# Performance work log

Measured on AMD Instinct MI355X. Metric: run time of the kernel, lower is better.

Reference implementation:

```python
import jax, jax.numpy as jnp
import numpy as np

N_NODES = 10000
N_EDGES = 160000
MUL = 16            # multiplicity: emb_dim=64, max_l=1 -> irreps 16x0e + 16x1o
EMB = 64
NUM_BASIS = 10
MAX_RADIUS = 4.5
HIDDEN = 64
N_PATHS = 4         # (0e,0e->0e), (0e,1o->1o), (1o,0e->1o), (1o,1o->0e)
W_NUMEL = N_PATHS * MUL * MUL  # 1024


def setup_inputs() -> dict:
    key = jax.random.key(0)
    ks = jax.random.split(key, 6)
    x = jax.random.normal(ks[0], (N_NODES, EMB), jnp.float32)
    src = jax.random.randint(ks[1], (N_EDGES,), 0, N_NODES)
    dst = jax.random.randint(ks[2], (N_EDGES,), 0, N_NODES)
    edge_vec = jax.random.normal(ks[3], (N_EDGES, 3), jnp.float32)
    mlp_w1 = jax.random.normal(ks[4], (NUM_BASIS, HIDDEN), jnp.float32)
    mlp_w2 = jax.random.normal(ks[5], (HIDDEN, W_NUMEL), jnp.float32)
    return {"x": x, "edge_vec": edge_vec, "mlp_w1": mlp_w1,
            "mlp_w2": mlp_w2, "src": src, "dst": dst}


def _sus(t):
    # e3nn smooth bump helper: exp(-1/t) for t>0 else 0
    return jnp.where(t > 0, jnp.exp(-1.0 / jnp.where(t > 0, t, 1.0)), 0.0)


def _radial_embedding(r):
    # soft_one_hot_linspace(basis='smooth_finite', cutoff=True), then *sqrt(num_basis)
    values = jnp.linspace(0.0, MAX_RADIUS, NUM_BASIS + 2)[1:-1]
    step = MAX_RADIUS / (NUM_BASIS + 1)
    diff = (r[:, None] - values) / step                     # [E, NUM_BASIS]
    basis = 1.14136 * jnp.exp(2.0) * _sus(diff + 1.0) * _sus(1.0 - diff)
    return basis * (NUM_BASIS ** 0.5)


def _forward(x, edge_vec, mlp_w1, mlp_w2, src, dst):
    E = edge_vec.shape[0]
    N = x.shape[0]
    r = jnp.linalg.norm(edge_vec, axis=1)                   # [E]
    # spherical harmonics, lmax=1, normalize=True, 'component' norm: Y0=1, Y1=sqrt(3)*n
    y1 = jnp.sqrt(3.0) * edge_vec / r[:, None]              # [E, 3]

    # radial MLP (e3nn FullyConnectedNet: W~N(0,1), x@W/sqrt(fan_in), relu scaled by sqrt(2))
    emb = _radial_embedding(r)                              # [E, 10]
    h = jnp.sqrt(2.0) * jax.nn.relu(emb @ (mlp_w1 / NUM_BASIS ** 0.5))
    w = h @ (mlp_w2 / HIDDEN ** 0.5)                        # [E, 1024]
    w = w.reshape(E, N_PATHS, MUL, MUL)                     # paths in e3nn order A,B,C,D

    xs = x[src]                                             # gather [E, 64]
    x0 = xs[:, :MUL]                                        # [E, 16] 0e scalars
    x1 = xs[:, MUL:].reshape(E, MUL, 3)                     # [E, 16, 3] 1o vectors

    # Fully connected TP normalization ('component', path_norm 'element'):
    # out0 fan = 2*MUL -> alpha 1/(2*MUL); out1 alpha 3/(2*MUL) with w3j 1/sqrt(3)
    c = 1.0 / jnp.sqrt(2.0 * MUL)
    inv_sqrt3 = 1.0 / jnp.sqrt(3.0)
    wA, wB, wC, wD = w[:, 0], w[:, 1], w[:, 2], w[:, 3]
    # 0e outputs: 0e*0e->0e and 1o*1o->0e (dot product, w3j = I/sqrt(3))
    out0 = c * (jnp.einsum('euw,eu->ew', wA, x0)
                + inv_sqrt3 * jnp.einsum('euw,eum,em->ew', wD, x1, y1))
    # 1o outputs: 0e*1o->1o and 1o*0e->1o (w3j = I/sqrt(3), Y0 = 1)
    out1 = c * (jnp.einsum('euw,eu,em->ewm', wB, x0, y1)
                + jnp.einsum('euw,eum->ewm', wC, x1))
    summand = jnp.concatenate([out0, out1.reshape(E, MUL * 3)], axis=1)  # [E, 64]

    out = jax.ops.segment_sum(summand, dst, num_segments=N)             # [N, 64]
    return out * (N / E)


def reference(x, edge_vec, mlp_w1, mlp_w2, src, dst):
    return _forward(x, edge_vec, mlp_w1, mlp_w2, src, dst)
```

## Files before the change

### kernel.cpp

```cpp
#include <hip/hip_runtime.h>
#include <hip/hip_bf16.h>


typedef __attribute__((ext_vector_type(8))) short bf16x8;
typedef __attribute__((ext_vector_type(4))) float f32x4;

#define NN 10000
#define NE 160000

__device__ __forceinline__ float sus_f(float t) { return t > 0.0f ? __expf(-1.0f / t) : 0.0f; }
__device__ __forceinline__ unsigned int f2bf(float f) {
    unsigned int u = __float_as_uint(f);
    u += 0x7FFFu + ((u >> 16) & 1u);
    return u >> 16;
}
__device__ __forceinline__ float bf2f(unsigned short v) { return __uint_as_float(((unsigned int)v) << 16); }

#define GL16(g, l) __builtin_amdgcn_global_load_lds( \
    (const __attribute__((address_space(1))) void*)(g), \
    (__attribute__((address_space(3))) void*)(l), 16, 0, 0)

__device__ __forceinline__ void stage_lds(const void* g, void* l, int bytes, int wv, int lane) {
    const char* gc = (const char*)g;
    char* lc = (char*)l;
    const int units = bytes >> 4;
    for (int u0 = wv << 6; u0 < units; u0 += 512) {
        if (u0 + lane < units) GL16(gc + (((long)(u0 + lane)) << 4), lc + (u0 << 4));
    }
}

__global__ void hist_k(const int* __restrict__ dst, int* __restrict__ hist,
                       const float* __restrict__ w2, char* __restrict__ w2bf) {
    if (blockIdx.x < 625) {
        const int e = blockIdx.x * 256 + threadIdx.x;
        if (e < NE) atomicAdd(&hist[dst[e]], 1);
    } else {
        const int idx = (blockIdx.x - 625) * 256 + threadIdx.x;
        const int j = idx >> 10, R = idx & 1023;
        unsigned int pk[4];
        #pragma unroll
        for (int p = 0; p < 4; ++p) {
            const unsigned int lo = f2bf(w2[(size_t)(8 * j + 2 * p) * 1024 + R]);
            const unsigned int hi = f2bf(w2[(size_t)(8 * j + 2 * p + 1) * 1024 + R]);
            pk[p] = lo | (hi << 16);
        }
        uint4 v; v.x = pk[0]; v.y = pk[1]; v.z = pk[2]; v.w = pk[3];
        *(uint4*)(w2bf + R * 128 + ((j ^ (R & 7)) << 4)) = v;
    }
}

__global__ __launch_bounds__(1024) void scan_k(const int* __restrict__ hist,
                                               int* __restrict__ offsets) {
    __shared__ int hl[NN];
    __shared__ int wsum[16];
    const int tid = threadIdx.x;
    for (int i = tid; i < NN; i += 1024) hl[i] = hist[i];
    __syncthreads();
    const int base = tid * 10;
    int loc[10]; int s = 0;
    #pragma unroll
    for (int i = 0; i < 10; ++i) { loc[i] = s; const int b = base + i; s += (b < NN) ? hl[b] : 0; }
    int v = s;
    const int lane = tid & 63, wv = tid >> 6;
    #pragma unroll
    for (int d = 1; d < 64; d <<= 1) { int t2 = __shfl_up(v, d); if (lane >= d) v += t2; }
    if (lane == 63) wsum[wv] = v;
    __syncthreads();
    if (tid < 64) {
        int w = (tid < 16) ? wsum[tid] : 0;
        #pragma unroll
        for (int d = 1; d < 16; d <<= 1) { int t2 = __shfl_up(w, d); if (tid >= d) w += t2; }
        if (tid < 16) wsum[tid] = w;
    }
    __syncthreads();
    const int wexc = (wv == 0) ? 0 : wsum[wv - 1];
    const int texc = wexc + v - s;
    #pragma unroll
    for (int i = 0; i < 10; ++i) { const int b = base + i; if (b < NN) offsets[b] = texc + loc[i]; }
    if (tid == 1023) offsets[NN] = texc + s;
}

__global__ void scatter_k(const int* __restrict__ dst, const int* __restrict__ offsets,
                          int* __restrict__ cursor, int* __restrict__ perm,
                          int* __restrict__ dsts) {
    const int e = blockIdx.x * 256 + threadIdx.x;
    if (e < NE) {
        const int d = dst[e];
        const int pos = offsets[d] + atomicAdd(&cursor[d], 1);
        perm[pos] = e;
        dsts[pos] = d;
    }
}

__global__ __launch_bounds__(256, 4) void prep_k(
    const float* __restrict__ x, const float* __restrict__ edge_vec,
    const float* __restrict__ w1, const int* __restrict__ src,
    const int* __restrict__ perm,
    char* __restrict__ h_bf, char* __restrict__ X0g, char* __restrict__ Zg,
    char* __restrict__ X1g, float* __restrict__ Y1g)
{
    __shared__ float embl[128][10];
    __shared__ float y1l[128][4];
    __shared__ int srcl[128];
    __shared__ float w1l[640];
    const int tid = threadIdx.x;
    const long e0 = (long)blockIdx.x * 128;

    for (int i = tid; i < 640; i += 256) w1l[i] = w1[i];
    if (tid < 128) {
        const int e = tid;
        const int eid = perm[e0 + e];
        const float vx = edge_vec[eid * 3 + 0];
        const float vy = edge_vec[eid * 3 + 1];
        const float vz = edge_vec[eid * 3 + 2];
        const float r = sqrtf(vx * vx + vy * vy + vz * vz);
        const float sc = 1.7320508075688772f / r;
        y1l[e][0] = vx * sc; y1l[e][1] = vy * sc; y1l[e][2] = vz * sc; y1l[e][3] = 0.f;
        *(float4*)&Y1g[(e0 + e) * 4] = make_float4(vx * sc, vy * sc, vz * sc, 0.f);
        srcl[e] = src[eid];
        const float C0 = 1.14136f * __expf(2.0f) * 3.1622776601683795f;
        #pragma unroll
        for (int i = 0; i < 10; ++i) {
            const float diff = r * (11.0f / 4.5f) - (float)(i + 1);
            embl[e][i] = C0 * sus_f(diff + 1.0f) * sus_f(1.0f - diff);
        }
    }
    __syncthreads();
    for (int idx = tid; idx < 1024; idx += 256) {
        const int e = idx >> 3, j = idx & 7;
        float acc[8];
        #pragma unroll
        for (int jj = 0; jj < 8; ++jj) acc[jj] = 0.0f;
        #pragma unroll
        for (int i = 0; i < 10; ++i) {
            const float ei = embl[e][i];
            #pragma unroll
            for (int jj = 0; jj < 8; ++jj) acc[jj] += ei * w1l[i * 64 + j * 8 + jj];
        }
        unsigned int pk[4];
        #pragma unroll
        for (int p = 0; p < 4; ++p) {
            const unsigned int lo = f2bf(fmaxf(acc[2 * p],     0.0f) * 0.4472135954999579f);
            const unsigned int hi = f2bf(fmaxf(acc[2 * p + 1], 0.0f) * 0.4472135954999579f);
            pk[p] = lo | (hi << 16);
        }
        uint4 v; v.x = pk[0]; v.y = pk[1]; v.z = pk[2]; v.w = pk[3];
        *(uint4*)(h_bf + (e0 + e) * 128 + ((j ^ (e & 7)) << 4)) = v;
    }
    for (int idx = tid; idx < 1024; idx += 256) {
        const int e = idx >> 3, p = idx & 7;
        const int s = srcl[e];
        const float2 ab = *(const float2*)&x[(size_t)s * 64 + 2 * p];
        *(unsigned int*)(X0g + (e0 + e) * 36 + p * 4) = f2bf(ab.x) | (f2bf(ab.y) << 16);
    }
    for (int idx = tid; idx < 1024; idx += 256) {
        const int e = idx >> 3, p = idx & 7;
        const int s = srcl[e];
        const float* xp = x + (size_t)s * 64 + 16 + 6 * p;
        const float z0 = xp[0] * y1l[e][0] + xp[1] * y1l[e][1] + xp[2] * y1l[e][2];
        const float z1 = xp[3] * y1l[e][0] + xp[4] * y1l[e][1] + xp[5] * y1l[e][2];
        *(unsigned int*)(Zg + (e0 + e) * 36 + p * 4) = f2bf(z0) | (f2bf(z1) << 16);
    }
    for (int idx = tid; idx < 128 * 12; idx += 256) {
        const int e = idx / 12, qd = idx - e * 12;
        const int s = srcl[e];
        const float4 v = *(const float4*)&x[(size_t)s * 64 + 16 + 4 * qd];
        *(float4*)(X1g + (e0 + e) * 208 + qd * 16) = v;
    }
}

#define BUF_SZ 48128

__global__ __launch_bounds__(512, 2) void se3_edge2(
    const char* __restrict__ w2bf, const char* __restrict__ h_bf,
    const char* __restrict__ X0g, const char* __restrict__ Zg,
    const char* __restrict__ X1g, const float* __restrict__ Y1g,
    const int* __restrict__ dsts, float* __restrict__ out)
{
    __shared__ __align__(16) char w2lds[65536];
    __shared__ __align__(16) char bufs[2][BUF_SZ];
    __shared__ int segst[2][66];
    __shared__ int nseg[2];

    const int tid = threadIdx.x, lane = tid & 63, wv = tid >> 6;
    const int lm = lane & 15, q = lane >> 4;
    const int bx = blockIdx.x;
    const int pair = (bx & 1) ^ ((bx >> 8) & 1);
    const int tb = bx >> 1;
    const int s0 = (q ^ (lm & 7)) << 4;
    const int s1 = s0 ^ 64;
    const int erow = wv << 4;

    const char* w2p0 = w2lds;
    const char* w2p1 = w2lds + 32768;
    {
        const int pa = pair ? 1 : 0, pb = pair ? 2 : 3;
        stage_lds(w2bf + pa * 32768, w2lds, 32768, wv, lane);
        stage_lds(w2bf + pb * 32768, w2lds + 32768, 32768, wv, lane);
        const long e0 = (long)tb * 5 * 128;
        stage_lds(h_bf + e0 * 128, bufs[0], 16384, wv, lane);
        stage_lds(X0g + e0 * 36, bufs[0] + 16384, 4608, wv, lane);
        if (pair) stage_lds(X1g + e0 * 208, bufs[0] + 20992, 26624, wv, lane);
        else      stage_lds(Zg  + e0 * 36,  bufs[0] + 20992, 4608,  wv, lane);
        stage_lds((const char*)(dsts + e0), bufs[0] + 47616, 512, wv, lane);
    }
    __syncthreads();

    const float S = 0.17677669529663687f * 0.125f * 0.0625f;

    for (int tt = 0; tt < 5; ++tt) {
        char* buf = bufs[tt & 1];
        const long gt = (long)tb * 5 + tt;
        const long e0 = gt * 128;
        if (tt < 4) {
            char* nb = bufs[(tt & 1) ^ 1];
            const long ne0 = e0 + 128;
            stage_lds(h_bf + ne0 * 128, nb, 16384, wv, lane);
            stage_lds(X0g + ne0 * 36, nb + 16384, 4608, wv, lane);
            if (pair) stage_lds(X1g + ne0 * 208, nb + 20992, 26624, wv, lane);
            else      stage_lds(Zg  + ne0 * 36,  nb + 20992, 4608,  wv, lane);
            stage_lds((const char*)(dsts + ne0), nb + 47616, 512, wv, lane);
        }
        const char* hl = buf;
        const int arow = erow + lm;
        const bf16x8 a0 = *(const bf16x8*)(hl + arow * 128 + s0);
        const bf16x8 a1 = *(const bf16x8*)(hl + arow * 128 + s1);
        const unsigned short* X0l = (const unsigned short*)(buf + 16384);
        const int* dstl = (const int*)(buf + 47616);

        float ac0[4] = {0,0,0,0}, ac1[4] = {0,0,0,0}, ac2[4] = {0,0,0,0}, ac3[4] = {0,0,0,0};

        if (pair == 0) {
            const unsigned short* Zl = (const unsigned short*)(buf + 20992);
            #pragma unroll 4
            for (int t = 0; t < 16; ++t) {
                const int rowb = (t * 16 + lm) << 7;
                const bf16x8 b00 = *(const bf16x8*)(w2p0 + rowb + s0);
                const bf16x8 b01 = *(const bf16x8*)(w2p0 + rowb + s1);
                const bf16x8 b10 = *(const bf16x8*)(w2p1 + rowb + s0);
                const bf16x8 b11 = *(const bf16x8*)(w2p1 + rowb + s1);
                f32x4 wA = {0.f,0.f,0.f,0.f};
                wA = __builtin_amdgcn_mfma_f32_16x16x32_bf16(a0, b00, wA, 0,0,0);
                wA = __builtin_amdgcn_mfma_f32_16x16x32_bf16(a1, b01, wA, 0,0,0);
                f32x4 wD = {0.f,0.f,0.f,0.f};
                wD = __builtin_amdgcn_mfma_f32_16x16x32_bf16(a0, b10, wD, 0,0,0);
                wD = __builtin_amdgcn_mfma_f32_16x16x32_bf16(a1, b11, wD, 0,0,0);
                #pragma unroll
                for (int r = 0; r < 4; ++r) {
                    const int el = erow + 4 * q + r;
                    ac0[r] += wA[r] * bf2f(X0l[el * 18 + t]);
                    ac1[r] += wD[r] * bf2f(Zl[el * 18 + t]);
                }
            }
            float* summ32 = (float*)buf;
            #pragma unroll
            for (int r = 0; r < 4; ++r) {
                const int el = erow + 4 * q + r;
                summ32[el * 17 + lm] = S * (ac0[r] + 0.5773502691896258f * ac1[r]);
            }
        } else {
            const float* X1l = (const float*)(buf + 20992);
            #pragma unroll 4
            for (int t = 0; t < 16; ++t) {
                const int rowb = (t * 16 + lm) << 7;
                const bf16x8 b00 = *(const bf16x8*)(w2p0 + rowb + s0);
                const bf16x8 b01 = *(const bf16x8*)(w2p0 + rowb + s1);
                const bf16x8 b10 = *(const bf16x8*)(w2p1 + rowb + s0);
                const bf16x8 b11 = *(const bf16x8*)(w2p1 + rowb + s1);
                f32x4 wB = {0.f,0.f,0.f,0.f};
                wB = __builtin_amdgcn_mfma_f32_16x16x32_bf16(a0, b00, wB, 0,0,0);
                wB = __builtin_amdgcn_mfma_f32_16x16x32_bf16(a1, b01, wB, 0,0,0);
                f32x4 wC = {0.f,0.f,0.f,0.f};
                wC = __builtin_amdgcn_mfma_f32_16x16x32_bf16(a0, b10, wC, 0,0,0);
                wC = __builtin_amdgcn_mfma_f32_16x16x32_bf16(a1, b11, wC, 0,0,0);
                #pragma unroll
                for (int r = 0; r < 4; ++r) {
                    const int el = erow + 4 * q + r;
                    ac0[r] += wB[r] * bf2f(X0l[el * 18 + t]);
                    ac1[r] += wC[r] * X1l[el * 52 + 3 * t + 0];
                    ac2[r] += wC[r] * X1l[el * 52 + 3 * t + 1];
                    ac3[r] += wC[r] * X1l[el * 52 + 3 * t + 2];
                }
            }
            unsigned short* summ16 = (unsigned short*)buf;
            #pragma unroll
            for (int r = 0; r < 4; ++r) {
                const int el = erow + 4 * q + r;
                const float4 y = *(const float4*)&Y1g[(e0 + el) * 4];
                const float b = S * ac0[r];
                summ16[el * 49 + 3 * lm + 0] = (unsigned short)f2bf(b * y.x + S * ac1[r]);
                summ16[el * 49 + 3 * lm + 1] = (unsigned short)f2bf(b * y.y + S * ac2[r]);
                summ16[el * 49 + 3 * lm + 2] = (unsigned short)f2bf(b * y.z + S * ac3[r]);
            }
        }
        if (wv < 2) {
            const int base = wv << 6;
            const int d = dstl[base + lane];
            const bool flag = (lane == 0) || (d != dstl[base + lane - 1]);
            const unsigned long long m = __ballot(flag);
            const int sid = (lane == 0) ? 0 : __popcll(m & ((1ull << lane) - 1ull));
            if (flag) segst[wv][sid] = base + lane;
            if (lane == 63) { const int ns = __popcll(m); nseg[wv] = ns; segst[wv][ns] = base + 64; }
        }
        __syncthreads();
        const int nsa = nseg[0], nsb = nseg[1];
        if (pair == 0) {
            const float* summ32 = (const float*)buf;
            const int total = (nsa + nsb) * 16;
            for (int i = tid; i < total; i += 512) {
                const int sg = i >> 4, c = i & 15;
                const int hh = sg >= nsa;
                const int sl = hh ? sg - nsa : sg;
                const int eb = segst[hh][sl], ee = segst[hh][sl + 1];
                float sum = 0.f;
                for (int e = eb; e < ee; ++e) sum += summ32[e * 17 + c];
                atomicAdd(&out[(size_t)dstl[eb] * 64 + c], sum);
            }
        } else {
            const unsigned short* summ16 = (const unsigned short*)buf;
            const int total = (nsa + nsb) * 48;
            for (int i = tid; i < total; i += 512) {
                const int sg = i / 48, c = i - sg * 48;
                const int hh = sg >= nsa;
                const int sl = hh ? sg - nsa : sg;
                const int eb = segst[hh][sl], ee = segst[hh][sl + 1];
                float sum = 0.f;
                for (int e = eb; e < ee; ++e) sum += bf2f(summ16[e * 49 + c]);
                atomicAdd(&out[(size_t)dstl[eb] * 64 + 16 + c], sum);
            }
        }
        __syncthreads();
    }
}

#define FBT 64
template<int PATH>
__device__ __forceinline__ void fb_body(
    const float* __restrict__ x, const float* __restrict__ edge_vec,
    const float* __restrict__ w1, const float* __restrict__ w2,
    const int* __restrict__ src, const int* __restrict__ perm,
    const int* __restrict__ dsts, float* __restrict__ out,
    unsigned short (*w2t)[72], float* arena, float (*y1l)[4],
    int* dstl, int* srcl, int* segstart, int* nseg_s)
{
    constexpr int NC    = (PATH == 0 || PATH == 3) ? 16 : 48;
    constexpr int CBASE = (PATH == 0 || PATH == 3) ? 0 : 16;
    const int tid = threadIdx.x;
    float* embl = arena;
    unsigned short* hl = (unsigned short*)(arena + 640);
    float* feats = arena + 2944;
    float* summ  = arena;
    {
        const float* col = w2 + PATH * 256 + tid;
        #pragma unroll
        for (int k = 0; k < 64; k += 2) {
            const unsigned int lo = f2bf(col[(size_t)k * 1024]);
            const unsigned int hi = f2bf(col[(size_t)(k + 1) * 1024]);
            *(unsigned int*)&w2t[tid][k] = lo | (hi << 16);
        }
    }
    const int lane = tid & 63, wv = tid >> 6, lm = lane & 15, q = lane >> 4;
    const int erow = wv * 16;
    const float C0 = 1.14136f * __expf(2.0f) * 3.1622776601683795f;
    const float S  = 0.17677669529663687f * 0.125f * 0.0625f;
    for (int it = 0; it < 2; ++it) {
        const int e0 = (blockIdx.x * 2 + it) * FBT;
        __syncthreads();
        for (int idx = tid; idx < FBT * 10; idx += 256) {
            const int e = idx / 10, i = idx - e * 10;
            const int eid = perm[e0 + e];
            const float vx = edge_vec[eid * 3 + 0], vy = edge_vec[eid * 3 + 1], vz = edge_vec[eid * 3 + 2];
            const float r = sqrtf(vx * vx + vy * vy + vz * vz);
            const float diff = r * (11.0f / 4.5f) - (float)(i + 1);
            embl[e * 10 + i] = C0 * sus_f(diff + 1.0f) * sus_f(1.0f - diff);
            if (i == 0) {
                const float sc = 1.7320508075688772f / r;
                y1l[e][0] = vx * sc; y1l[e][1] = vy * sc; y1l[e][2] = vz * sc;
                dstl[e] = dsts[e0 + e];
                srcl[e] = src[eid];
            }
        }
        __syncthreads();
        for (int idx = tid; idx < FBT * 8; idx += 256) {
            const int e = idx >> 3, j0 = (idx & 7) * 8;
            float acc[8];
            #pragma unroll
            for (int j = 0; j < 8; ++j) acc[j] = 0.0f;
            #pragma unroll
            for (int i = 0; i < 10; ++i) {
                const float ei = embl[e * 10 + i];
                #pragma unroll
                for (int j = 0; j < 8; ++j) acc[j] += ei * w1[i * 64 + j0 + j];
            }
            unsigned int pk[4];
            #pragma unroll
            for (int p = 0; p < 4; ++p) {
                const unsigned int lo = f2bf(fmaxf(acc[2 * p],     0.0f) * 0.4472135954999579f);
                const unsigned int hi = f2bf(fmaxf(acc[2 * p + 1], 0.0f) * 0.4472135954999579f);
                pk[p] = lo | (hi << 16);
            }
            uint4 v; v.x = pk[0]; v.y = pk[1]; v.z = pk[2]; v.w = pk[3];
            *(uint4*)&hl[e * 72 + j0] = v;
        }
        if (PATH == 2) {
            for (int idx = tid; idx < FBT * 48; idx += 256) {
                const int e = idx / 48, c = idx - e * 48;
                feats[e * 48 + c] = x[(size_t)srcl[e] * 64 + 16 + c];
            }
        } else if (PATH == 3) {
            for (int idx = tid; idx < FBT * 16; idx += 256) {
                const int e = idx >> 4, u = idx & 15;
                const float* xs = x + (size_t)srcl[e] * 64 + 16 + u * 3;
                feats[e * 16 + u] = xs[0] * y1l[e][0] + xs[1] * y1l[e][1] + xs[2] * y1l[e][2];
            }
        } else {
            for (int idx = tid; idx < FBT * 16; idx += 256) {
                const int e = idx >> 4, u = idx & 15;
                feats[e * 16 + u] = x[(size_t)srcl[e] * 64 + u];
            }
        }
        __syncthreads();
        const bf16x8 a0 = *(const bf16x8*)&hl[(erow + lm) * 72 + 8 * q];
        const bf16x8 a1 = *(const bf16x8*)&hl[(erow + lm) * 72 + 32 + 8 * q];
        float accO[4] = {0.f,0.f,0.f,0.f}, accC0[4] = {0.f,0.f,0.f,0.f};
        float accC1[4] = {0.f,0.f,0.f,0.f}, accC2[4] = {0.f,0.f,0.f,0.f};
        #pragma unroll 4
        for (int t = 0; t < 16; ++t) {
            const bf16x8 b0 = *(const bf16x8*)&w2t[t * 16 + lm][8 * q];
            const bf16x8 b1 = *(const bf16x8*)&w2t[t * 16 + lm][32 + 8 * q];
            f32x4 wa = {0.f,0.f,0.f,0.f};
            wa = __builtin_amdgcn_mfma_f32_16x16x32_bf16(a0, b0, wa, 0, 0, 0);
            wa = __builtin_amdgcn_mfma_f32_16x16x32_bf16(a1, b1, wa, 0, 0, 0);
            #pragma unroll
            for (int r = 0; r < 4; ++r) {
                const int el = erow + 4 * q + r;
                if (PATH == 2) {
                    accC0[r] += wa[r] * feats[el * 48 + t * 3 + 0];
                    accC1[r] += wa[r] * feats[el * 48 + t * 3 + 1];
                    accC2[r] += wa[r] * feats[el * 48 + t * 3 + 2];
                } else {
                    accO[r] += wa[r] * feats[el * 16 + t];
                }
            }
        }
        __syncthreads();
        #pragma unroll
        for (int r = 0; r < 4; ++r) {
            const int el = erow + 4 * q + r;
            if (PATH == 0) summ[el * 16 + lm] = S * accO[r];
            else if (PATH == 3) summ[el * 16 + lm] = S * 0.5773502691896258f * accO[r];
            else if (PATH == 1) {
                const float tv = S * accO[r];
                summ[el * 48 + lm * 3 + 0] = tv * y1l[el][0];
                summ[el * 48 + lm * 3 + 1] = tv * y1l[el][1];
                summ[el * 48 + lm * 3 + 2] = tv * y1l[el][2];
            } else {
                summ[el * 48 + lm * 3 + 0] = S * accC0[r];
                summ[el * 48 + lm * 3 + 1] = S * accC1[r];
                summ[el * 48 + lm * 3 + 2] = S * accC2[r];
            }
        }
        if (tid < 64) {
            const int d = dstl[tid];
            const bool flag = (tid == 0) || (d != dstl[tid - 1]);
            const unsigned long long m = __ballot(flag);
            const int sid = (tid == 0) ? 0 : __popcll(m & ((1ull << tid) - 1ull));
            if (flag) segstart[sid] = tid;
            if (tid == 63) { const int ns = __popcll(m); *nseg_s = ns; segstart[ns] = 64; }
        }
        __syncthreads();
        const int ns = *nseg_s;
        for (int i = tid; i < ns * NC; i += 256) {
            const int s = i / NC, c = i - s * NC;
            const int eb = segstart[s], ee = segstart[s + 1];
            float sum = 0.0f;
            for (int e = eb; e < ee; ++e) sum += summ[e * NC + c];
            atomicAdd(&out[(size_t)dstl[eb] * 64 + CBASE + c], sum);
        }
    }
}

__global__ __launch_bounds__(256, 2) void fb_edge(
    const float* __restrict__ x, const float* __restrict__ edge_vec,
    const float* __restrict__ w1, const float* __restrict__ w2,
    const int* __restrict__ src, const int* __restrict__ perm,
    const int* __restrict__ dsts, float* __restrict__ out)
{
    __shared__ unsigned short w2t[256][72];
    __shared__ float arena[6016];
    __shared__ float y1l[FBT][4];
    __shared__ int dstl[FBT];
    __shared__ int srcl[FBT];
    __shared__ int segstart[FBT + 1];
    __shared__ int nseg_s;
    switch (blockIdx.y) {
        case 0:  fb_body<0>(x, edge_vec, w1, w2, src, perm, dsts, out, w2t, arena, y1l, dstl, srcl, segstart, &nseg_s); break;
        case 1:  fb_body<1>(x, edge_vec, w1, w2, src, perm, dsts, out, w2t, arena, y1l, dstl, srcl, segstart, &nseg_s); break;
        case 2:  fb_body<2>(x, edge_vec, w1, w2, src, perm, dsts, out, w2t, arena, y1l, dstl, srcl, segstart, &nseg_s); break;
        default: fb_body<3>(x, edge_vec, w1, w2, src, perm, dsts, out, w2t, arena, y1l, dstl, srcl, segstart, &nseg_s); break;
    }
}

extern "C" void kernel_launch(void* const* d_in, const int* in_sizes, int n_in,
                              void* d_out, int out_size, void* d_ws, size_t ws_size,
                              hipStream_t stream) {
    const float* x        = (const float*)d_in[0];
    const float* edge_vec = (const float*)d_in[1];
    const float* w1       = (const float*)d_in[2];
    const float* w2       = (const float*)d_in[3];
    const int*   src      = (const int*)d_in[4];
    const int*   dst      = (const int*)d_in[5];
    float* out = (float*)d_out;

    char* ws = (char*)d_ws;
    size_t off = 0;
    auto alloc = [&](size_t n) -> char* {
        off = (off + 255) & ~(size_t)255;
        char* p = ws + off; off += n; return p;
    };
    int* hist    = (int*)alloc(40000);
    int* cursor  = (int*)alloc(40000);
    int* offsets = (int*)alloc(40004);
    int* perm    = (int*)alloc(640000);
    int* dsts    = (int*)alloc(640000);
    char* w2bf   = alloc(131072);
    char* h_bf   = alloc((size_t)NE * 128);
    char* X0g    = alloc((size_t)NE * 36);
    char* Zg     = alloc((size_t)NE * 36);
    float* Y1g   = (float*)alloc((size_t)NE * 16);
    char* X1g    = alloc((size_t)NE * 208);
    const bool big = (off <= ws_size);

    hipMemsetAsync(d_out, 0, (size_t)out_size * sizeof(float), stream);
    hipMemsetAsync(d_ws, 0, 81408, stream);

    if (big) {
        hipLaunchKernelGGL(hist_k, dim3(657), dim3(256), 0, stream, dst, hist, w2, w2bf);
        hipLaunchKernelGGL(scan_k, dim3(1), dim3(1024), 0, stream, hist, offsets);
        hipLaunchKernelGGL(scatter_k, dim3(625), dim3(256), 0, stream, dst, offsets, cursor, perm, dsts);
        hipLaunchKernelGGL(prep_k, dim3(1250), dim3(256), 0, stream,
                           x, edge_vec, w1, src, perm, h_bf, X0g, Zg, X1g, Y1g);
        hipLaunchKernelGGL(se3_edge2, dim3(500), dim3(512), 0, stream,
                           w2bf, h_bf, X0g, Zg, X1g, Y1g, dsts, out);
    } else {
        hipLaunchKernelGGL(hist_k, dim3(625), dim3(256), 0, stream, dst, hist, w2, w2bf);
        hipLaunchKernelGGL(scan_k, dim3(1), dim3(1024), 0, stream, hist, offsets);
        hipLaunchKernelGGL(scatter_k, dim3(625), dim3(256), 0, stream, dst, offsets, cursor, perm, dsts);
        hipLaunchKernelGGL(fb_edge, dim3(1250, 4), dim3(256), 0, stream,
                           x, edge_vec, w1, w2, src, perm, dsts, out);
    }
}
```

Measured before the change: 126.8 us.

## Fuse scatter into prep, compact staged layouts, split edge kernel across 1024 threads

Removes the separate scatter kernel: prep now iterates edges in original order, computes each edge's sorted position with an atomic cursor and writes its per-edge data directly to that position. The staged per-edge buffers lose their padding (X0/Z at 32 bytes, X1 stored as bf16 at 128 bytes), and Y1 is staged into LDS. The main edge kernel goes from 512 to 1024 threads per block, splitting the 16 weight tiles across two wave halves with an LDS reduction before the segmented atomic scatter. This cuts global traffic and a launch, at the cost of scattered writes in prep, an extra barrier round, and bf16 rounding of X1.

```diff
diff --git a/kernel.cpp b/kernel.cpp
--- a/kernel.cpp
+++ b/kernel.cpp
@@ -3,6 +3,7 @@
 
 
 typedef __attribute__((ext_vector_type(8))) short bf16x8;
+typedef __attribute__((ext_vector_type(8))) unsigned short u16x8;
 typedef __attribute__((ext_vector_type(4))) float f32x4;
 
 #define NN 10000
@@ -15,18 +16,19 @@
     return u >> 16;
 }
 __device__ __forceinline__ float bf2f(unsigned short v) { return __uint_as_float(((unsigned int)v) << 16); }
+__device__ __forceinline__ float bflo(unsigned int v) { return __uint_as_float(v << 16); }
+__device__ __forceinline__ float bfhi(unsigned int v) { return __uint_as_float(v & 0xFFFF0000u); }
+__device__ __forceinline__ float bfe(u16x8 v, int i) { return __uint_as_float(((unsigned int)v[i]) << 16); }
 
 #define GL16(g, l) __builtin_amdgcn_global_load_lds( \
     (const __attribute__((address_space(1))) void*)(g), \
     (__attribute__((address_space(3))) void*)(l), 16, 0, 0)
 
-__device__ __forceinline__ void stage_lds(const void* g, void* l, int bytes, int wv, int lane) {
+__device__ __forceinline__ void stageN(const void* g, void* l, int bytes, int tid, int nthr) {
     const char* gc = (const char*)g;
     char* lc = (char*)l;
     const int units = bytes >> 4;
-    for (int u0 = wv << 6; u0 < units; u0 += 512) {
-        if (u0 + lane < units) GL16(gc + (((long)(u0 + lane)) << 4), lc + (u0 << 4));
-    }
+    for (int u = tid; u < units; u += nthr) GL16(gc + ((long)u << 4), lc + (u << 4));
 }
 
 __global__ void hist_k(const int* __restrict__ dst, int* __restrict__ hist,
@@ -80,6 +82,288 @@
     if (tid == 1023) offsets[NN] = texc + s;
 }
 
+__global__ __launch_bounds__(256, 4) void prep_k(
+    const float* __restrict__ x, const float* __restrict__ edge_vec,
+    const float* __restrict__ w1, const int* __restrict__ src,
+    const int* __restrict__ dst, const int* __restrict__ offsets,
+    int* __restrict__ cursor, int* __restrict__ dsts,
+    char* __restrict__ h_bf, char* __restrict__ X0g, char* __restrict__ Zg,
+    char* __restrict__ X1g, float* __restrict__ Y1g)
+{
+    __shared__ float embl[128][10];
+    __shared__ float y1l[128][4];
+    __shared__ int srcl[128];
+    __shared__ int posl[128];
+    __shared__ float w1l[640];
+    const int tid = threadIdx.x;
+    const int e0 = blockIdx.x * 128;
+
+    for (int i = tid; i < 640; i += 256) w1l[i] = w1[i];
+    if (tid < 128) {
+        const int eid = e0 + tid;
+        const int d = dst[eid];
+        const int pos = offsets[d] + atomicAdd(&cursor[d], 1);
+        posl[tid] = pos;
+        dsts[pos] = d;
+        const float vx = edge_vec[eid * 3 + 0];
+        const float vy = edge_vec[eid * 3 + 1];
+        const float vz = edge_vec[eid * 3 + 2];
+        const float r = sqrtf(vx * vx + vy * vy + vz * vz);
+        const float sc = 1.7320508075688772f / r;
+        y1l[tid][0] = vx * sc; y1l[tid][1] = vy * sc; y1l[tid][2] = vz * sc; y1l[tid][3] = 0.f;
+        *(float4*)&Y1g[(size_t)pos * 4] = make_float4(vx * sc, vy * sc, vz * sc, 0.f);
+        srcl[tid] = src[eid];
+        const float C0 = 1.14136f * __expf(2.0f) * 3.1622776601683795f;
+        #pragma unroll
+        for (int i = 0; i < 10; ++i) {
+            const float diff = r * (11.0f / 4.5f) - (float)(i + 1);
+            embl[tid][i] = C0 * sus_f(diff + 1.0f) * sus_f(1.0f - diff);
+        }
+    }
+    __syncthreads();
+    for (int idx = tid; idx < 1024; idx += 256) {
+        const int e = idx >> 3, j = idx & 7;
+        float acc[8];
+        #pragma unroll
+        for (int jj = 0; jj < 8; ++jj) acc[jj] = 0.0f;
+        #pragma unroll
+        for (int i = 0; i < 10; ++i) {
+            const float ei = embl[e][i];
+            #pragma unroll
+            for (int jj = 0; jj < 8; ++jj) acc[jj] += ei * w1l[i * 64 + j * 8 + jj];
+        }
+        unsigned int pk[4];
+        #pragma unroll
+        for (int p = 0; p < 4; ++p) {
+            const unsigned int lo = f2bf(fmaxf(acc[2 * p],     0.0f) * 0.4472135954999579f);
+            const unsigned int hi = f2bf(fmaxf(acc[2 * p + 1], 0.0f) * 0.4472135954999579f);
+            pk[p] = lo | (hi << 16);
+        }
+        const int pos = posl[e];
+        uint4 v; v.x = pk[0]; v.y = pk[1]; v.z = pk[2]; v.w = pk[3];
+        *(uint4*)(h_bf + (size_t)pos * 128 + ((j ^ (pos & 7)) << 4)) = v;
+    }
+    for (int idx = tid; idx < 1024; idx += 256) {
+        const int e = idx >> 3, p = idx & 7;
+        const int s = srcl[e];
+        const float2 ab = *(const float2*)&x[(size_t)s * 64 + 2 * p];
+        *(unsigned int*)(X0g + (size_t)posl[e] * 32 + p * 4) = f2bf(ab.x) | (f2bf(ab.y) << 16);
+    }
+    for (int idx = tid; idx < 1024; idx += 256) {
+        const int e = idx >> 3, p = idx & 7;
+        const int s = srcl[e];
+        const float* xp = x + (size_t)s * 64 + 16 + 6 * p;
+        const float z0 = xp[0] * y1l[e][0] + xp[1] * y1l[e][1] + xp[2] * y1l[e][2];
+        const float z1 = xp[3] * y1l[e][0] + xp[4] * y1l[e][1] + xp[5] * y1l[e][2];
+        *(unsigned int*)(Zg + (size_t)posl[e] * 32 + p * 4) = f2bf(z0) | (f2bf(z1) << 16);
+    }
+    for (int idx = tid; idx < 2048; idx += 256) {
+        const int e = idx >> 4, u = idx & 15;
+        const int s = srcl[e];
+        const float* xp = x + (size_t)s * 64 + 16 + 3 * u;
+        uint2 v;
+        v.x = f2bf(xp[0]) | (f2bf(xp[1]) << 16);
+        v.y = f2bf(xp[2]);
+        *(uint2*)(X1g + (size_t)posl[e] * 128 + u * 8) = v;
+    }
+}
+
+#define BUF 43520
+
+__global__ __launch_bounds__(1024, 4) void se3_edge3(
+    const char* __restrict__ w2bf, const char* __restrict__ h_bf,
+    const char* __restrict__ X0g, const char* __restrict__ Zg,
+    const char* __restrict__ X1g, const float* __restrict__ Y1g,
+    const int* __restrict__ dsts, float* __restrict__ out)
+{
+    __shared__ __align__(16) char w2lds[65536];
+    __shared__ __align__(16) char bufs[2][BUF];
+    __shared__ int segst[2][66];
+    __shared__ int nseg[2];
+
+    const int tid = threadIdx.x, lane = tid & 63, wv = tid >> 6;
+    const int lm = lane & 15, q = lane >> 4;
+    const int g = wv & 7, th = wv >> 3;
+    const int erow = g << 4;
+    const int bx = blockIdx.x;
+    const int pair = bx & 1;
+    const int tb = bx >> 1;
+    const int s0 = (q ^ (lm & 7)) << 4;
+    const int s1 = s0 ^ 64;
+
+    const char* w2p0 = w2lds;
+    const char* w2p1 = w2lds + 32768;
+
+    auto stage_tile = [&](char* nb, long e0) {
+        stageN(h_bf + e0 * 128, nb, 16384, tid, 1024);
+        stageN(X0g + e0 * 32, nb + 16384, 4096, tid, 1024);
+        if (pair) {
+            stageN(X1g + e0 * 128, nb + 24576, 16384, tid, 1024);
+            stageN((const char*)(Y1g + e0 * 4), nb + 40960, 2048, tid, 1024);
+        } else {
+            stageN(Zg + e0 * 32, nb + 20480, 4096, tid, 1024);
+        }
+        stageN((const char*)(dsts + e0), nb + 43008, 512, tid, 1024);
+    };
+
+    {
+        const int pa = pair ? 1 : 0, pb = pair ? 2 : 3;
+        stageN(w2bf + pa * 32768, w2lds, 32768, tid, 1024);
+        stageN(w2bf + pb * 32768, w2lds + 32768, 32768, tid, 1024);
+        stage_tile(bufs[0], (long)tb * 5 * 128);
+    }
+    __syncthreads();
+
+    const float S = 0.17677669529663687f * 0.125f * 0.0625f;
+
+    for (int tt = 0; tt < 5; ++tt) {
+        char* buf = bufs[tt & 1];
+        const long e0 = ((long)tb * 5 + tt) * 128;
+        if (tt < 4) stage_tile(bufs[(tt & 1) ^ 1], e0 + 128);
+
+        const int arow = erow + lm;
+        const bf16x8 a0 = *(const bf16x8*)(buf + arow * 128 + s0);
+        const bf16x8 a1 = *(const bf16x8*)(buf + arow * 128 + s1);
+        u16x8 x0r[4], zr[4];
+        #pragma unroll
+        for (int r = 0; r < 4; ++r) {
+            const int el = erow + 4 * q + r;
+            x0r[r] = *(const u16x8*)(buf + 16384 + el * 32 + th * 16);
+            if (pair == 0) zr[r] = *(const u16x8*)(buf + 20480 + el * 32 + th * 16);
+        }
+
+        float ac0[4] = {0,0,0,0}, ac1[4] = {0,0,0,0}, ac2[4] = {0,0,0,0}, ac3[4] = {0,0,0,0};
+        #pragma unroll
+        for (int tl = 0; tl < 8; ++tl) {
+            const int t = (th << 3) + tl;
+            const int rowb = (t * 16 + lm) << 7;
+            const bf16x8 b00 = *(const bf16x8*)(w2p0 + rowb + s0);
+            const bf16x8 b01 = *(const bf16x8*)(w2p0 + rowb + s1);
+            const bf16x8 b10 = *(const bf16x8*)(w2p1 + rowb + s0);
+            const bf16x8 b11 = *(const bf16x8*)(w2p1 + rowb + s1);
+            f32x4 w0 = {0.f,0.f,0.f,0.f}, w1v = {0.f,0.f,0.f,0.f};
+            w0 = __builtin_amdgcn_mfma_f32_16x16x32_bf16(a0, b00, w0, 0,0,0);
+            w0 = __builtin_amdgcn_mfma_f32_16x16x32_bf16(a1, b01, w0, 0,0,0);
+            w1v = __builtin_amdgcn_mfma_f32_16x16x32_bf16(a0, b10, w1v, 0,0,0);
+            w1v = __builtin_amdgcn_mfma_f32_16x16x32_bf16(a1, b11, w1v, 0,0,0);
+            if (pair == 0) {
+                #pragma unroll
+                for (int r = 0; r < 4; ++r) {
+                    ac0[r] += w0[r] * bfe(x0r[r], tl);
+                    ac1[r] += w1v[r] * bfe(zr[r], tl);
+                }
+            } else {
+                #pragma unroll
+                for (int r = 0; r < 4; ++r) {
+                    const int el = erow + 4 * q + r;
+                    const uint2 xv = *(const uint2*)(buf + 24576 + (el * 16 + t) * 8);
+                    ac0[r] += w0[r] * bfe(x0r[r], tl);
+                    ac1[r] += w1v[r] * bflo(xv.x);
+                    ac2[r] += w1v[r] * bfhi(xv.x);
+                    ac3[r] += w1v[r] * bflo(xv.y);
+                }
+            }
+        }
+        __syncthreads();
+
+        if (th == 1) {
+            char* pb = buf + (g * 64 + lane) * 32;
+            if (pair == 0) {
+                *(float4*)pb = make_float4(ac0[0], ac0[1], ac0[2], ac0[3]);
+                *(float4*)(pb + 16) = make_float4(ac1[0], ac1[1], ac1[2], ac1[3]);
+            } else {
+                uint4 v0, v1;
+                v0.x = f2bf(ac0[0]) | (f2bf(ac0[1]) << 16);
+                v0.y = f2bf(ac0[2]) | (f2bf(ac0[3]) << 16);
+                v0.z = f2bf(ac1[0]) | (f2bf(ac1[1]) << 16);
+                v0.w = f2bf(ac1[2]) | (f2bf(ac1[3]) << 16);
+                v1.x = f2bf(ac2[0]) | (f2bf(ac2[1]) << 16);
+                v1.y = f2bf(ac2[2]) | (f2bf(ac2[3]) << 16);
+                v1.z = f2bf(ac3[0]) | (f2bf(ac3[1]) << 16);
+                v1.w = f2bf(ac3[2]) | (f2bf(ac3[3]) << 16);
+                *(uint4*)pb = v0;
+                *(uint4*)(pb + 16) = v1;
+            }
+        }
+        __syncthreads();
+
+        if (th == 0) {
+            const char* pb = buf + (g * 64 + lane) * 32;
+            if (pair == 0) {
+                const float4 p0 = *(const float4*)pb;
+                const float4 p1 = *(const float4*)(pb + 16);
+                float* sm = (float*)(buf + 16384);
+                #pragma unroll
+                for (int r = 0; r < 4; ++r) {
+                    const int el = erow + 4 * q + r;
+                    const float a = ac0[r] + ((const float*)&p0)[r];
+                    const float d = ac1[r] + ((const float*)&p1)[r];
+                    sm[lm * 129 + el] = S * (a + 0.5773502691896258f * d);
+                }
+            } else {
+                const uint4 v0 = *(const uint4*)pb;
+                const uint4 v1 = *(const uint4*)(pb + 16);
+                const float pB[4]  = { bflo(v0.x), bfhi(v0.x), bflo(v0.y), bfhi(v0.y) };
+                const float pC0[4] = { bflo(v0.z), bfhi(v0.z), bflo(v0.w), bfhi(v0.w) };
+                const float pC1[4] = { bflo(v1.x), bfhi(v1.x), bflo(v1.y), bfhi(v1.y) };
+                const float pC2[4] = { bflo(v1.z), bfhi(v1.z), bflo(v1.w), bfhi(v1.w) };
+                unsigned short* sm = (unsigned short*)(buf + 16384);
+                #pragma unroll
+                for (int r = 0; r < 4; ++r) {
+                    const int el = erow + 4 * q + r;
+                    const float4 y = *(const float4*)(buf + 40960 + el * 16);
+                    const float b  = S * (ac0[r] + pB[r]);
+                    const float c0 = S * (ac1[r] + pC0[r]);
+                    const float c1 = S * (ac2[r] + pC1[r]);
+                    const float c2 = S * (ac3[r] + pC2[r]);
+                    sm[(3 * lm + 0) * 130 + el] = (unsigned short)f2bf(b * y.x + c0);
+                    sm[(3 * lm + 1) * 130 + el] = (unsigned short)f2bf(b * y.y + c1);
+                    sm[(3 * lm + 2) * 130 + el] = (unsigned short)f2bf(b * y.z + c2);
+                }
+            }
+        }
+        const int* dstl = (const int*)(buf + 43008);
+        if (wv < 2) {
+            const int base = wv << 6;
+            const int d = dstl[base + lane];
+            const bool flag = (lane == 0) || (d != dstl[base + lane - 1]);
+            const unsigned long long m = __ballot(flag);
+            const int sid = (lane == 0) ? 0 : __popcll(m & ((1ull << lane) - 1ull));
+            if (flag) segst[wv][sid] = base + lane;
+            if (lane == 63) { const int ns = __popcll(m); nseg[wv] = ns; segst[wv][ns] = base + 64; }
+        }
+        __syncthreads();
+
+        const int nsa = nseg[0], nsb = nseg[1];
+        if (pair == 0) {
+            const float* sm = (const float*)(buf + 16384);
+            const int total = (nsa + nsb) << 4;
+            for (int i = tid; i < total; i += 1024) {
+                const int sg = i >> 4, c = i & 15;
+                const int hh = (sg >= nsa) ? 1 : 0;
+                const int sl = hh ? sg - nsa : sg;
+                const int eb = segst[hh][sl], ee = segst[hh][sl + 1];
+                float s = 0.f;
+                for (int e = eb; e < ee; ++e) s += sm[c * 129 + e];
+                atomicAdd(&out[(size_t)dstl[eb] * 64 + c], s);
+            }
+        } else {
+            const unsigned short* sm = (const unsigned short*)(buf + 16384);
+            const int total = (nsa + nsb) * 48;
+            for (int i = tid; i < total; i += 1024) {
+                const int sg = i / 48, c = i - sg * 48;
+                const int hh = (sg >= nsa) ? 1 : 0;
+                const int sl = hh ? sg - nsa : sg;
+                const int eb = segst[hh][sl], ee = segst[hh][sl + 1];
+                float s = 0.f;
+                for (int e = eb; e < ee; ++e) s += bf2f(sm[c * 130 + e]);
+                atomicAdd(&out[(size_t)dstl[eb] * 64 + 16 + c], s);
+            }
+        }
+        __syncthreads();
+    }
+}
+
 __global__ void scatter_k(const int* __restrict__ dst, const int* __restrict__ offsets,
                           int* __restrict__ cursor, int* __restrict__ perm,
                           int* __restrict__ dsts) {
@@ -89,247 +373,6 @@
         const int pos = offsets[d] + atomicAdd(&cursor[d], 1);
         perm[pos] = e;
         dsts[pos] = d;
-    }
-}
-
-__global__ __launch_bounds__(256, 4) void prep_k(
-    const float* __restrict__ x, const float* __restrict__ edge_vec,
-    const float* __restrict__ w1, const int* __restrict__ src,
-    const int* __restrict__ perm,
-    char* __restrict__ h_bf, char* __restrict__ X0g, char* __restrict__ Zg,
-    char* __restrict__ X1g, float* __restrict__ Y1g)
-{
-    __shared__ float embl[128][10];
-    __shared__ float y1l[128][4];
-    __shared__ int srcl[128];
-    __shared__ float w1l[640];
-    const int tid = threadIdx.x;
-    const long e0 = (long)blockIdx.x * 128;
-
-    for (int i = tid; i < 640; i += 256) w1l[i] = w1[i];
-    if (tid < 128) {
-        const int e = tid;
-        const int eid = perm[e0 + e];
-        const float vx = edge_vec[eid * 3 + 0];
-        const float vy = edge_vec[eid * 3 + 1];
-        const float vz = edge_vec[eid * 3 + 2];
-        const float r = sqrtf(vx * vx + vy * vy + vz * vz);
-        const float sc = 1.7320508075688772f / r;
-        y1l[e][0] = vx * sc; y1l[e][1] = vy * sc; y1l[e][2] = vz * sc; y1l[e][3] = 0.f;
-        *(float4*)&Y1g[(e0 + e) * 4] = make_float4(vx * sc, vy * sc, vz * sc, 0.f);
-        srcl[e] = src[eid];
-        const float C0 = 1.14136f * __expf(2.0f) * 3.1622776601683795f;
-        #pragma unroll
-        for (int i = 0; i < 10; ++i) {
-            const float diff = r * (11.0f / 4.5f) - (float)(i + 1);
-            embl[e][i] = C0 * sus_f(diff + 1.0f) * sus_f(1.0f - diff);
-        }
-    }
-    __syncthreads();
-    for (int idx = tid; idx < 1024; idx += 256) {
-        const int e = idx >> 3, j = idx & 7;
-        float acc[8];
-        #pragma unroll
-        for (int jj = 0; jj < 8; ++jj) acc[jj] = 0.0f;
-        #pragma unroll
-        for (int i = 0; i < 10; ++i) {
-            const float ei = embl[e][i];
-            #pragma unroll
-            for (int jj = 0; jj < 8; ++jj) acc[jj] += ei * w1l[i * 64 + j * 8 + jj];
-        }
-        unsigned int pk[4];
-        #pragma unroll
-        for (int p = 0; p < 4; ++p) {
-            const unsigned int lo = f2bf(fmaxf(acc[2 * p],     0.0f) * 0.4472135954999579f);
-            const unsigned int hi = f2bf(fmaxf(acc[2 * p + 1], 0.0f) * 0.4472135954999579f);
-            pk[p] = lo | (hi << 16);
-        }
-        uint4 v; v.x = pk[0]; v.y = pk[1]; v.z = pk[2]; v.w = pk[3];
-        *(uint4*)(h_bf + (e0 + e) * 128 + ((j ^ (e & 7)) << 4)) = v;
-    }
-    for (int idx = tid; idx < 1024; idx += 256) {
-        const int e = idx >> 3, p = idx & 7;
-        const int s = srcl[e];
-        const float2 ab = *(const float2*)&x[(size_t)s * 64 + 2 * p];
-        *(unsigned int*)(X0g + (e0 + e) * 36 + p * 4) = f2bf(ab.x) | (f2bf(ab.y) << 16);
-    }
-    for (int idx = tid; idx < 1024; idx += 256) {
-        const int e = idx >> 3, p = idx & 7;
-        const int s = srcl[e];
-        const float* xp = x + (size_t)s * 64 + 16 + 6 * p;
-        const float z0 = xp[0] * y1l[e][0] + xp[1] * y1l[e][1] + xp[2] * y1l[e][2];
-        const float z1 = xp[3] * y1l[e][0] + xp[4] * y1l[e][1] + xp[5] * y1l[e][2];
-        *(unsigned int*)(Zg + (e0 + e) * 36 + p * 4) = f2bf(z0) | (f2bf(z1) << 16);
-    }
-    for (int idx = tid; idx < 128 * 12; idx += 256) {
-        const int e = idx / 12, qd = idx - e * 12;
-        const int s = srcl[e];
-        const float4 v = *(const float4*)&x[(size_t)s * 64 + 16 + 4 * qd];
-        *(float4*)(X1g + (e0 + e) * 208 + qd * 16) = v;
-    }
-}
-
-#define BUF_SZ 48128
-
-__global__ __launch_bounds__(512, 2) void se3_edge2(
-    const char* __restrict__ w2bf, const char* __restrict__ h_bf,
-    const char* __restrict__ X0g, const char* __restrict__ Zg,
-    const char* __restrict__ X1g, const float* __restrict__ Y1g,
-    const int* __restrict__ dsts, float* __restrict__ out)
-{
-    __shared__ __align__(16) char w2lds[65536];
-    __shared__ __align__(16) char bufs[2][BUF_SZ];
-    __shared__ int segst[2][66];
-    __shared__ int nseg[2];
-
-    const int tid = threadIdx.x, lane = tid & 63, wv = tid >> 6;
-    const int lm = lane & 15, q = lane >> 4;
-    const int bx = blockIdx.x;
-    const int pair = (bx & 1) ^ ((bx >> 8) & 1);
-    const int tb = bx >> 1;
-    const int s0 = (q ^ (lm & 7)) << 4;
-    const int s1 = s0 ^ 64;
-    const int erow = wv << 4;
-
-    const char* w2p0 = w2lds;
-    const char* w2p1 = w2lds + 32768;
-    {
-        const int pa = pair ? 1 : 0, pb = pair ? 2 : 3;
-        stage_lds(w2bf + pa * 32768, w2lds, 32768, wv, lane);
-        stage_lds(w2bf + pb * 32768, w2lds + 32768, 32768, wv, lane);
-        const long e0 = (long)tb * 5 * 128;
-        stage_lds(h_bf + e0 * 128, bufs[0], 16384, wv, lane);
-        stage_lds(X0g + e0 * 36, bufs[0] + 16384, 4608, wv, lane);
-        if (pair) stage_lds(X1g + e0 * 208, bufs[0] + 20992, 26624, wv, lane);
-        else      stage_lds(Zg  + e0 * 36,  bufs[0] + 20992, 4608,  wv, lane);
-        stage_lds((const char*)(dsts + e0), bufs[0] + 47616, 512, wv, lane);
-    }
-    __syncthreads();
-
-    const float S = 0.17677669529663687f * 0.125f * 0.0625f;
-
-    for (int tt = 0; tt < 5; ++tt) {
-        char* buf = bufs[tt & 1];
-        const long gt = (long)tb * 5 + tt;
-        const long e0 = gt * 128;
-        if (tt < 4) {
-            char* nb = bufs[(tt & 1) ^ 1];
-            const long ne0 = e0 + 128;
-            stage_lds(h_bf + ne0 * 128, nb, 16384, wv, lane);
-            stage_lds(X0g + ne0 * 36, nb + 16384, 4608, wv, lane);
-            if (pair) stage_lds(X1g + ne0 * 208, nb + 20992, 26624, wv, lane);
-            else      stage_lds(Zg  + ne0 * 36,  nb + 20992, 4608,  wv, lane);
-            stage_lds((const char*)(dsts + ne0), nb + 47616, 512, wv, lane);
-        }
-        const char* hl = buf;
-        const int arow = erow + lm;
-        const bf16x8 a0 = *(const bf16x8*)(hl + arow * 128 + s0);
-        const bf16x8 a1 = *(const bf16x8*)(hl + arow * 128 + s1);
-        const unsigned short* X0l = (const unsigned short*)(buf + 16384);
-        const int* dstl = (const int*)(buf + 47616);
-
-        float ac0[4] = {0,0,0,0}, ac1[4] = {0,0,0,0}, ac2[4] = {0,0,0,0}, ac3[4] = {0,0,0,0};
-
-        if (pair == 0) {
-            const unsigned short* Zl = (const unsigned short*)(buf + 20992);
-            #pragma unroll 4
-            for (int t = 0; t < 16; ++t) {
-                const int rowb = (t * 16 + lm) << 7;
-                const bf16x8 b00 = *(const bf16x8*)(w2p0 + rowb + s0);
-                const bf16x8 b01 = *(const bf16x8*)(w2p0 + rowb + s1);
-                const bf16x8 b10 = *(const bf16x8*)(w2p1 + rowb + s0);
-                const bf16x8 b11 = *(const bf16x8*)(w2p1 + rowb + s1);
-                f32x4 wA = {0.f,0.f,0.f,0.f};
-                wA = __builtin_amdgcn_mfma_f32_16x16x32_bf16(a0, b00, wA, 0,0,0);
-                wA = __builtin_amdgcn_mfma_f32_16x16x32_bf16(a1, b01, wA, 0,0,0);
-                f32x4 wD = {0.f,0.f,0.f,0.f};
-                wD = __builtin_amdgcn_mfma_f32_16x16x32_bf16(a0, b10, wD, 0,0,0);
-                wD = __builtin_amdgcn_mfma_f32_16x16x32_bf16(a1, b11, wD, 0,0,0);
-                #pragma unroll
-                for (int r = 0; r < 4; ++r) {
-                    const int el = erow + 4 * q + r;
-                    ac0[r] += wA[r] * bf2f(X0l[el * 18 + t]);
-                    ac1[r] += wD[r] * bf2f(Zl[el * 18 + t]);
-                }
-            }
-            float* summ32 = (float*)buf;
-            #pragma unroll
-            for (int r = 0; r < 4; ++r) {
-                const int el = erow + 4 * q + r;
-                summ32[el * 17 + lm] = S * (ac0[r] + 0.5773502691896258f * ac1[r]);
-            }
-        } else {
-            const float* X1l = (const float*)(buf + 20992);
-            #pragma unroll 4
-            for (int t = 0; t < 16; ++t) {
-                const int rowb = (t * 16 + lm) << 7;
-                const bf16x8 b00 = *(const bf16x8*)(w2p0 + rowb + s0);
-                const bf16x8 b01 = *(const bf16x8*)(w2p0 + rowb + s1);
-                const bf16x8 b10 = *(const bf16x8*)(w2p1 + rowb + s0);
-                const bf16x8 b11 = *(const bf16x8*)(w2p1 + rowb + s1);
-                f32x4 wB = {0.f,0.f,0.f,0.f};
-                wB = __builtin_amdgcn_mfma_f32_16x16x32_bf16(a0, b00, wB, 0,0,0);
-                wB = __builtin_amdgcn_mfma_f32_16x16x32_bf16(a1, b01, wB, 0,0,0);
-                f32x4 wC = {0.f,0.f,0.f,0.f};
-                wC = __builtin_amdgcn_mfma_f32_16x16x32_bf16(a0, b10, wC, 0,0,0);
-                wC = __builtin_amdgcn_mfma_f32_16x16x32_bf16(a1, b11, wC, 0,0,0);
-                #pragma unroll
-                for (int r = 0; r < 4; ++r) {
-                    const int el = erow + 4 * q + r;
-                    ac0[r] += wB[r] * bf2f(X0l[el * 18 + t]);
-                    ac1[r] += wC[r] * X1l[el * 52 + 3 * t + 0];
-                    ac2[r] += wC[r] * X1l[el * 52 + 3 * t + 1];
-                    ac3[r] += wC[r] * X1l[el * 52 + 3 * t + 2];
-                }
-            }
-            unsigned short* summ16 = (unsigned short*)buf;
-            #pragma unroll
-            for (int r = 0; r < 4; ++r) {
-                const int el = erow + 4 * q + r;
-                const float4 y = *(const float4*)&Y1g[(e0 + el) * 4];
-                const float b = S * ac0[r];
-                summ16[el * 49 + 3 * lm + 0] = (unsigned short)f2bf(b * y.x + S * ac1[r]);
-                summ16[el * 49 + 3 * lm + 1] = (unsigned short)f2bf(b * y.y + S * ac2[r]);
-                summ16[el * 49 + 3 * lm + 2] = (unsigned short)f2bf(b * y.z + S * ac3[r]);
-            }
-        }
-        if (wv < 2) {
-            const int base = wv << 6;
-            const int d = dstl[base + lane];
-            const bool flag = (lane == 0) || (d != dstl[base + lane - 1]);
-            const unsigned long long m = __ballot(flag);
-            const int sid = (lane == 0) ? 0 : __popcll(m & ((1ull << lane) - 1ull));
-            if (flag) segst[wv][sid] = base + lane;
-            if (lane == 63) { const int ns = __popcll(m); nseg[wv] = ns; segst[wv][ns] = base + 64; }
-        }
-        __syncthreads();
-        const int nsa = nseg[0], nsb = nseg[1];
-        if (pair == 0) {
-            const float* summ32 = (const float*)buf;
-            const int total = (nsa + nsb) * 16;
-            for (int i = tid; i < total; i += 512) {
-                const int sg = i >> 4, c = i & 15;
-                const int hh = sg >= nsa;
-                const int sl = hh ? sg - nsa : sg;
-                const int eb = segst[hh][sl], ee = segst[hh][sl + 1];
-                float sum = 0.f;
-                for (int e = eb; e < ee; ++e) sum += summ32[e * 17 + c];
-                atomicAdd(&out[(size_t)dstl[eb] * 64 + c], sum);
-            }
-        } else {
-            const unsigned short* summ16 = (const unsigned short*)buf;
-            const int total = (nsa + nsb) * 48;
-            for (int i = tid; i < total; i += 512) {
-                const int sg = i / 48, c = i - sg * 48;
-                const int hh = sg >= nsa;
-                const int sl = hh ? sg - nsa : sg;
-                const int eb = segst[hh][sl], ee = segst[hh][sl + 1];
-                float sum = 0.f;
-                for (int e = eb; e < ee; ++e) sum += bf2f(summ16[e * 49 + c]);
-                atomicAdd(&out[(size_t)dstl[eb] * 64 + 16 + c], sum);
-            }
-        }
-        __syncthreads();
     }
 }
 
@@ -525,10 +568,10 @@
     int* dsts    = (int*)alloc(640000);
     char* w2bf   = alloc(131072);
     char* h_bf   = alloc((size_t)NE * 128);
-    char* X0g    = alloc((size_t)NE * 36);
-    char* Zg     = alloc((size_t)NE * 36);
+    char* X0g    = alloc((size_t)NE * 32);
+    char* Zg     = alloc((size_t)NE * 32);
+    char* X1g    = alloc((size_t)NE * 128);
     float* Y1g   = (float*)alloc((size_t)NE * 16);
-    char* X1g    = alloc((size_t)NE * 208);
     const bool big = (off <= ws_size);
 
     hipMemsetAsync(d_out, 0, (size_t)out_size * sizeof(float), stream);
@@ -537,10 +580,10 @@
     if (big) {
         hipLaunchKernelGGL(hist_k, dim3(657), dim3(256), 0, stream, dst, hist, w2, w2bf);
         hipLaunchKernelGGL(scan_k, dim3(1), dim3(1024), 0, stream, hist, offsets);
-        hipLaunchKernelGGL(scatter_k, dim3(625), dim3(256), 0, stream, dst, offsets, cursor, perm, dsts);
         hipLaunchKernelGGL(prep_k, dim3(1250), dim3(256), 0, stream,
-                           x, edge_vec, w1, src, perm, h_bf, X0g, Zg, X1g, Y1g);
-        hipLaunchKernelGGL(se3_edge2, dim3(500), dim3(512), 0, stream,
+                           x, edge_vec, w1, src, dst, offsets, cursor, dsts,
+                           h_bf, X0g, Zg, X1g, Y1g);
+        hipLaunchKernelGGL(se3_edge3, dim3(500), dim3(1024), 0, stream,
                            w2bf, h_bf, X0g, Zg, X1g, Y1g, dsts, out);
     } else {
         hipLaunchKernelGGL(hist_k, dim3(625), dim3(256), 0, stream, dst, hist, w2, w2bf);
```

Measured after the change: 146.2 us. 15.3% more time.
